# Kernel tuning notes

Hardware: AMD Instinct MI355X
Metric: run time of the kernel (lower is better)

## Reference

```python
import jax, jax.numpy as jnp
import numpy as np

B, L, D = 4, 8192, 1024

def setup_inputs() -> dict:
    key = jax.random.key(0)
    kx, kg, kc = jax.random.split(key, 3)
    scale = 1.0 / np.sqrt(D)  # ~xavier for [D,D]
    return {
        "x": jax.random.normal(kx, (B, L, D), dtype=jnp.float32),
        "Wg": jax.random.normal(kg, (D, D), dtype=jnp.float32) * scale,
        "bg": jnp.ones((D,), dtype=jnp.float32),   # gate bias init = 1.0
        "Wc": jax.random.normal(kc, (D, D), dtype=jnp.float32) * scale,
        "bc": jnp.zeros((D,), dtype=jnp.float32),  # candidate bias init = 0
    }

def _mingru_scan(gates, candidates):
    # Linear recurrence h_t = g_t * h_{t-1} + c_t, h_0 = 0, along axis=1 (L).
    # Associative combine for pairs (a, b) representing h -> a*h + b.
    def combine(e1, e2):
        a1, b1 = e1
        a2, b2 = e2
        return a2 * a1, a2 * b1 + b2
    _, h = jax.lax.associative_scan(combine, (gates, candidates), axis=1)
    return h

def reference(x, Wg, bg, Wc, bc):
    # gate_proj / candidate_proj: y = x @ W.T + b (torch Linear convention)
    gates = jax.nn.sigmoid(jnp.einsum('bld,ed->ble', x, Wg) + bg)
    candidates = jnp.tanh(jnp.einsum('bld,ed->ble', x, Wc) + bc)
    return _mingru_scan(gates, candidates)  # dropout=0 -> identity
```

## Files before the change

kernel.cpp:

```cpp
#include <hip/hip_runtime.h>
#include <math.h>

#define B_ 4
#define L_ 8192
#define D_ 1024
#define M_ (B_ * L_)
#define K_ D_

#define BM 128
#define BN 128
#define BK 32

#define NCH 64
#define CHL 128

typedef short bf16x8 __attribute__((ext_vector_type(8)));
typedef float f32x4 __attribute__((ext_vector_type(4)));

__device__ __forceinline__ unsigned short f2bf(float f) {
    unsigned u = __float_as_uint(f);
    u += 0x7fff + ((u >> 16) & 1);
    return (unsigned short)(u >> 16);
}
__device__ __forceinline__ float bf2f(unsigned short h) {
    return __uint_as_float(((unsigned)h) << 16);
}

__device__ __forceinline__ void async16(const void* g, void* l) {
    __builtin_amdgcn_global_load_lds(
        (const __attribute__((address_space(1))) unsigned int*)g,
        (__attribute__((address_space(3))) unsigned int*)l, 16, 0, 0);
}

__global__ __launch_bounds__(256) void wprep_kernel(
    const float* __restrict__ Wg, const float* __restrict__ Wc,
    unsigned short* __restrict__ Wghi, unsigned short* __restrict__ Wglo,
    unsigned short* __restrict__ Wchi, unsigned short* __restrict__ Wclo)
{
    int idx = (blockIdx.x * 256 + threadIdx.x) * 4;
    const int n = D_ * D_;
    const float* src; unsigned short *dh, *dl; int o;
    if (idx < n) { src = Wg; dh = Wghi; dl = Wglo; o = idx; }
    else         { src = Wc; dh = Wchi; dl = Wclo; o = idx - n; }
    float4 v = *(const float4*)(src + o);
    ushort4 hi, lo;
    hi.x = f2bf(v.x); lo.x = f2bf(v.x - bf2f(hi.x));
    hi.y = f2bf(v.y); lo.y = f2bf(v.y - bf2f(hi.y));
    hi.z = f2bf(v.z); lo.z = f2bf(v.z - bf2f(hi.z));
    hi.w = f2bf(v.w); lo.w = f2bf(v.w - bf2f(hi.w));
    *(ushort4*)(dh + o) = hi;
    *(ushort4*)(dl + o) = lo;
}

__global__ __launch_bounds__(256, 2) void gemm_scan_kernel(
    const float* __restrict__ X,
    const unsigned short* __restrict__ Wghi, const unsigned short* __restrict__ Wglo,
    const unsigned short* __restrict__ Wchi, const unsigned short* __restrict__ Wclo,
    const float* __restrict__ bg, const float* __restrict__ bc,
    float* __restrict__ P_ws, float* __restrict__ h_ws,
    float* __restrict__ carryA, float* __restrict__ carryB)
{
    __shared__ __align__(16) unsigned short sAhi[BM * BK];
    __shared__ __align__(16) unsigned short sAlo[BM * BK];
    __shared__ __align__(16) unsigned short sB[2][4][BN * BK];

    const int t = threadIdx.x;
    const int lane = t & 63;
    const int w = t >> 6;
    const int wrow = w >> 1;
    const int wcol = w & 1;
    const int quad = lane >> 4;
    const int l16  = lane & 15;

    const int m0 = blockIdx.x * BM;
    const int n0 = blockIdx.y * BN;

    const int rsw = (((l16 & 3) ^ ((l16 >> 2) & 3)) << 3);
    const int kq  = (quad << 3) ^ rsw;
    const int aws = ((((t >> 3) & 3) ^ ((t >> 5) & 3)) << 3);
    const int bSrcChunk = (((t & 3) ^ ((t >> 2) & 3) ^ ((t >> 4) & 3)) << 3);

    const unsigned short* const wp[4] = {Wghi, Wglo, Wchi, Wclo};

    f32x4 accg[4][4] = {};
    f32x4 accc[4][4] = {};

#pragma unroll
    for (int p = 0; p < 2; ++p) {
        const int o   = t * 16 + p * 4096;
        const int row = (t >> 2) + p * 64;
        const size_t goff = (size_t)(n0 + row) * K_ + 0 + bSrcChunk;
#pragma unroll
        for (int pl = 0; pl < 4; ++pl)
            async16(wp[pl] + goff, (char*)sB[0][pl] + o);
    }

#pragma unroll 1
    for (int s = 0; s < 32; ++s) {
        const int k0  = s * BK;
        const int cur = s & 1;

        asm volatile("" ::: "memory");
        __builtin_amdgcn_s_barrier();
        asm volatile("" ::: "memory");

        float4 xv[4];
#pragma unroll
        for (int p = 0; p < 4; ++p) {
            const int row = p * 32 + (t >> 3);
            const int k   = (t & 7) * 4;
            xv[p] = *(const float4*)(X + (size_t)(m0 + row) * K_ + k0 + k);
        }

        if (s < 31) {
#pragma unroll
            for (int p = 0; p < 2; ++p) {
                const int o   = t * 16 + p * 4096;
                const int row = (t >> 2) + p * 64;
                const size_t goff = (size_t)(n0 + row) * K_ + (k0 + BK) + bSrcChunk;
#pragma unroll
                for (int pl = 0; pl < 4; ++pl)
                    async16(wp[pl] + goff, (char*)sB[cur ^ 1][pl] + o);
            }
        }

#pragma unroll
        for (int p = 0; p < 4; ++p) {
            const int row = p * 32 + (t >> 3);
            const int kk  = ((t & 7) * 4) ^ aws;
            float4 v = xv[p];
            ushort4 hi, lo;
            hi.x = f2bf(v.x); lo.x = f2bf(v.x - bf2f(hi.x));
            hi.y = f2bf(v.y); lo.y = f2bf(v.y - bf2f(hi.y));
            hi.z = f2bf(v.z); lo.z = f2bf(v.z - bf2f(hi.z));
            hi.w = f2bf(v.w); lo.w = f2bf(v.w - bf2f(hi.w));
            *(ushort4*)(sAhi + row * BK + kk) = hi;
            *(ushort4*)(sAlo + row * BK + kk) = lo;
        }

        asm volatile("s_waitcnt lgkmcnt(0)" ::: "memory");
        asm volatile("s_waitcnt vmcnt(8)" ::: "memory");
        __builtin_amdgcn_sched_barrier(0);

        __builtin_amdgcn_s_barrier();
        asm volatile("" ::: "memory");

        const unsigned short* __restrict__ sb0 = sB[cur][0];
        const unsigned short* __restrict__ sb1 = sB[cur][1];
        const unsigned short* __restrict__ sb2 = sB[cur][2];
        const unsigned short* __restrict__ sb3 = sB[cur][3];

        bf16x8 ahi[4], alo[4];
#pragma unroll
        for (int i = 0; i < 4; ++i) {
            const int off = (wrow * 64 + i * 16 + l16) * BK + kq;
            ahi[i] = *(const bf16x8*)(sAhi + off);
            alo[i] = *(const bf16x8*)(sAlo + off);
        }
#pragma unroll
        for (int j = 0; j < 4; ++j) {
            const int off = (wcol * 64 + j * 16 + l16) * BK + kq;
            bf16x8 bgh = *(const bf16x8*)(sb0 + off);
            bf16x8 bgl = *(const bf16x8*)(sb1 + off);
            bf16x8 bch = *(const bf16x8*)(sb2 + off);
            bf16x8 bcl = *(const bf16x8*)(sb3 + off);
#pragma unroll
            for (int i = 0; i < 4; ++i) {
                accg[i][j] = __builtin_amdgcn_mfma_f32_16x16x32_bf16(ahi[i], bgh, accg[i][j], 0, 0, 0);
                accg[i][j] = __builtin_amdgcn_mfma_f32_16x16x32_bf16(ahi[i], bgl, accg[i][j], 0, 0, 0);
                accg[i][j] = __builtin_amdgcn_mfma_f32_16x16x32_bf16(alo[i], bgh, accg[i][j], 0, 0, 0);
                accc[i][j] = __builtin_amdgcn_mfma_f32_16x16x32_bf16(ahi[i], bch, accc[i][j], 0, 0, 0);
                accc[i][j] = __builtin_amdgcn_mfma_f32_16x16x32_bf16(ahi[i], bcl, accc[i][j], 0, 0, 0);
                accc[i][j] = __builtin_amdgcn_mfma_f32_16x16x32_bf16(alo[i], bch, accc[i][j], 0, 0, 0);
            }
        }
    }

    const int b   = m0 >> 13;
    const int chk = (m0 & (L_ - 1)) >> 7;

    float RunA[4], RunB[4];
#pragma unroll
    for (int j = 0; j < 4; ++j) {
        const int n = n0 + wcol * 64 + j * 16 + l16;
        const float bgv = bg[n];
        const float bcv = bc[n];
        float Ar = 1.f, Br = 0.f;
#pragma unroll
        for (int i = 0; i < 4; ++i) {
            float P[4], H[4];
            float pp = 1.f, ph = 0.f;
#pragma unroll
            for (int r = 0; r < 4; ++r) {
                float zg = accg[i][j][r] + bgv;
                float zc = accc[i][j][r] + bcv;
                float g = 1.f / (1.f + __expf(-zg));
                float c = tanhf(zc);
                float Pv = (r == 0) ? g : g * pp;
                float Hv = (r == 0) ? c : fmaf(g, ph, c);
                P[r] = Pv; H[r] = Hv; pp = Pv; ph = Hv;
            }
            float Ai = P[3], Bi = H[3];
            float A1 = __shfl(Ai, (lane - 16) & 63);
            float B1 = __shfl(Bi, (lane - 16) & 63);
            if (quad >= 1) { Bi = fmaf(Ai, B1, Bi); Ai *= A1; }
            float A2 = __shfl(Ai, (lane - 32) & 63);
            float B2 = __shfl(Bi, (lane - 32) & 63);
            if (quad >= 2) { Bi = fmaf(Ai, B2, Bi); Ai *= A2; }
            float Ae = __shfl(Ai, (lane - 16) & 63);
            float Be = __shfl(Bi, (lane - 16) & 63);
            if (quad == 0) { Ae = 1.f; Be = 0.f; }
            float Ca = Ae * Ar;
            float Cb = fmaf(Ae, Br, Be);
#pragma unroll
            for (int r = 0; r < 4; ++r) {
                float Pr = P[r];
                accg[i][j][r] = Pr * Ca;
                accc[i][j][r] = fmaf(Pr, Cb, H[r]);
            }
            float Ag  = __shfl(Ai, l16 + 48);
            float Bg2 = __shfl(Bi, l16 + 48);
            Br = fmaf(Ag, Br, Bg2);
            Ar *= Ag;
        }
        RunA[j] = Ar; RunB[j] = Br;
    }

    __syncthreads();
    float* cwf = (float*)sAhi;

    if (wrow == 0 && quad == 0) {
#pragma unroll
        for (int j = 0; j < 4; ++j) {
            cwf[(((wcol * 4 + j) * 16 + l16) << 1) + 0] = RunA[j];
            cwf[(((wcol * 4 + j) * 16 + l16) << 1) + 1] = RunB[j];
        }
    }
    __syncthreads();
    if (wrow == 1) {
#pragma unroll
        for (int j = 0; j < 4; ++j) {
            float Aw = cwf[(((wcol * 4 + j) * 16 + l16) << 1) + 0];
            float Bw = cwf[(((wcol * 4 + j) * 16 + l16) << 1) + 1];
#pragma unroll
            for (int i = 0; i < 4; ++i) {
#pragma unroll
                for (int r = 0; r < 4; ++r) {
                    float Pe = accg[i][j][r];
                    accc[i][j][r] = fmaf(Pe, Bw, accc[i][j][r]);
                    accg[i][j][r] = Pe * Aw;
                }
            }
            if (quad == 0) {
                const int n = n0 + wcol * 64 + j * 16 + l16;
                size_t co = (((size_t)b * NCH + chk) << 10) + n;
                carryA[co] = RunA[j] * Aw;
                carryB[co] = fmaf(RunA[j], Bw, RunB[j]);
            }
        }
    }

#pragma unroll
    for (int j = 0; j < 4; ++j) {
        const int n = n0 + wcol * 64 + j * 16 + l16;
#pragma unroll
        for (int i = 0; i < 4; ++i) {
#pragma unroll
            for (int r = 0; r < 4; ++r) {
                int m = m0 + wrow * 64 + i * 16 + quad * 4 + r;
                size_t o = ((size_t)m << 10) + n;
                P_ws[o] = accg[i][j][r];
                h_ws[o] = accc[i][j][r];
            }
        }
    }
}

__global__ __launch_bounds__(256) void scan_carry_kernel(
    const float* __restrict__ carryA, float* __restrict__ carryB)
{
    const int idx = blockIdx.x * 256 + threadIdx.x;
    const int b = idx >> 10;
    const int d = idx & (D_ - 1);
    float acc = 0.f;
    for (int k = 0; k < NCH; ++k) {
        const size_t o = (((size_t)b * NCH + k) << 10) + d;
        const float a  = carryA[o];
        const float bb = carryB[o];
        carryB[o] = acc;
        acc = fmaf(a, acc, bb);
    }
}

__global__ __launch_bounds__(256) void scan_apply_kernel(
    const float* __restrict__ P_ws, const float* __restrict__ h_ws,
    const float* __restrict__ carryB, float* __restrict__ out)
{
    const size_t o = ((size_t)blockIdx.x * 256 + threadIdx.x) * 4;
    const int m  = (int)(o >> 10);
    const int d  = (int)(o & (D_ - 1));
    const int b  = m >> 13;
    const int ch = (m & (L_ - 1)) >> 7;
    const float4 hin = *(const float4*)(carryB + ((((size_t)b * NCH + ch) << 10) + d));
    const float4 P = *(const float4*)(P_ws + o);
    const float4 H = *(const float4*)(h_ws + o);
    float4 r;
    r.x = fmaf(P.x, hin.x, H.x);
    r.y = fmaf(P.y, hin.y, H.y);
    r.z = fmaf(P.z, hin.z, H.z);
    r.w = fmaf(P.w, hin.w, H.w);
    *(float4*)(out + o) = r;
}

extern "C" void kernel_launch(void* const* d_in, const int* in_sizes, int n_in,
                              void* d_out, int out_size, void* d_ws, size_t ws_size,
                              hipStream_t stream)
{
    const float* x  = (const float*)d_in[0];
    const float* Wg = (const float*)d_in[1];
    const float* bg = (const float*)d_in[2];
    const float* Wc = (const float*)d_in[3];
    const float* bc = (const float*)d_in[4];
    float* out = (float*)d_out;

    float* ws = (float*)d_ws;
    float* P_ws   = ws;
    float* h_ws   = P_ws + (size_t)M_ * D_;
    float* carryA = h_ws + (size_t)M_ * D_;
    float* carryB = carryA + (size_t)B_ * NCH * D_;
    unsigned short* Wghi = (unsigned short*)(carryB + (size_t)B_ * NCH * D_);
    unsigned short* Wglo = Wghi + (size_t)D_ * D_;
    unsigned short* Wchi = Wglo + (size_t)D_ * D_;
    unsigned short* Wclo = Wchi + (size_t)D_ * D_;

    wprep_kernel<<<(2 * D_ * D_ / 4) / 256, 256, 0, stream>>>(
        Wg, Wc, Wghi, Wglo, Wchi, Wclo);

    gemm_scan_kernel<<<dim3(M_ / BM, D_ / BN), 256, 0, stream>>>(
        x, Wghi, Wglo, Wchi, Wclo, bg, bc, P_ws, h_ws, carryA, carryB);

    scan_carry_kernel<<<(B_ * D_) / 256, 256, 0, stream>>>(carryA, carryB);

    scan_apply_kernel<<<(M_ * (D_ / 4)) / 256, 256, 0, stream>>>(
        P_ws, h_ws, carryB, out);
}
```

Baseline: 696.9 us.

## Pre-split X into bf16 hi/lo planes and stream A tiles via async copies

Adds an xprep kernel that splits X into bf16 hi/lo planes once, staged in the output buffer, so the GEMM loads A tiles with async global-to-LDS copies instead of per-tile fp32 register loads plus in-loop conversion. It removes the LDS swizzles, restructures B double-buffering with pointer swaps, and raises wave priority around the MFMA block. The cost is an extra full pass over X (read 128MB, write 128MB). Dropping the swizzle may add LDS bank conflicts, and the A tile is still loaded synchronously within each iteration rather than prefetched.

```diff
diff --git a/kernel.cpp b/kernel.cpp
--- a/kernel.cpp
+++ b/kernel.cpp
@@ -52,8 +52,23 @@
     *(ushort4*)(dl + o) = lo;
 }
 
+__global__ __launch_bounds__(256) void xprep_kernel(
+    const float* __restrict__ X,
+    unsigned short* __restrict__ Xhi, unsigned short* __restrict__ Xlo)
+{
+    size_t idx = ((size_t)blockIdx.x * 256 + threadIdx.x) * 4;
+    float4 v = *(const float4*)(X + idx);
+    ushort4 hi, lo;
+    hi.x = f2bf(v.x); lo.x = f2bf(v.x - bf2f(hi.x));
+    hi.y = f2bf(v.y); lo.y = f2bf(v.y - bf2f(hi.y));
+    hi.z = f2bf(v.z); lo.z = f2bf(v.z - bf2f(hi.z));
+    hi.w = f2bf(v.w); lo.w = f2bf(v.w - bf2f(hi.w));
+    *(ushort4*)(Xhi + idx) = hi;
+    *(ushort4*)(Xlo + idx) = lo;
+}
+
 __global__ __launch_bounds__(256, 2) void gemm_scan_kernel(
-    const float* __restrict__ X,
+    const unsigned short* __restrict__ Xhi, const unsigned short* __restrict__ Xlo,
     const unsigned short* __restrict__ Wghi, const unsigned short* __restrict__ Wglo,
     const unsigned short* __restrict__ Wchi, const unsigned short* __restrict__ Wclo,
     const float* __restrict__ bg, const float* __restrict__ bc,
@@ -75,95 +90,73 @@
     const int m0 = blockIdx.x * BM;
     const int n0 = blockIdx.y * BN;
 
-    const int rsw = (((l16 & 3) ^ ((l16 >> 2) & 3)) << 3);
-    const int kq  = (quad << 3) ^ rsw;
-    const int aws = ((((t >> 3) & 3) ^ ((t >> 5) & 3)) << 3);
-    const int bSrcChunk = (((t & 3) ^ ((t >> 2) & 3) ^ ((t >> 4) & 3)) << 3);
-
-    const unsigned short* const wp[4] = {Wghi, Wglo, Wchi, Wclo};
+    const int stRow = t >> 2;
+    const int stKc  = (t & 3) << 3;
+    const int stO   = t * 16;
 
     f32x4 accg[4][4] = {};
     f32x4 accc[4][4] = {};
 
+    unsigned short* sBc = &sB[0][0][0];
+    unsigned short* sBn = &sB[1][0][0];
+
 #pragma unroll
     for (int p = 0; p < 2; ++p) {
-        const int o   = t * 16 + p * 4096;
-        const int row = (t >> 2) + p * 64;
-        const size_t goff = (size_t)(n0 + row) * K_ + 0 + bSrcChunk;
-#pragma unroll
-        for (int pl = 0; pl < 4; ++pl)
-            async16(wp[pl] + goff, (char*)sB[0][pl] + o);
+        const int o = stO + p * 4096;
+        const size_t gb = (size_t)(n0 + stRow + p * 64) * K_ + stKc;
+        async16(Wghi + gb, (char*)sBc + o);
+        async16(Wglo + gb, (char*)sBc + 8192 + o);
+        async16(Wchi + gb, (char*)sBc + 16384 + o);
+        async16(Wclo + gb, (char*)sBc + 24576 + o);
     }
 
 #pragma unroll 1
     for (int s = 0; s < 32; ++s) {
-        const int k0  = s * BK;
-        const int cur = s & 1;
-
-        asm volatile("" ::: "memory");
+        const int k0 = s * BK;
+
         __builtin_amdgcn_s_barrier();
-        asm volatile("" ::: "memory");
-
-        float4 xv[4];
-#pragma unroll
-        for (int p = 0; p < 4; ++p) {
-            const int row = p * 32 + (t >> 3);
-            const int k   = (t & 7) * 4;
-            xv[p] = *(const float4*)(X + (size_t)(m0 + row) * K_ + k0 + k);
+
+#pragma unroll
+        for (int p = 0; p < 2; ++p) {
+            const int o = stO + p * 4096;
+            const size_t ga = (size_t)(m0 + stRow + p * 64) * K_ + k0 + stKc;
+            async16(Xhi + ga, (char*)sAhi + o);
+            async16(Xlo + ga, (char*)sAlo + o);
         }
 
         if (s < 31) {
 #pragma unroll
             for (int p = 0; p < 2; ++p) {
-                const int o   = t * 16 + p * 4096;
-                const int row = (t >> 2) + p * 64;
-                const size_t goff = (size_t)(n0 + row) * K_ + (k0 + BK) + bSrcChunk;
-#pragma unroll
-                for (int pl = 0; pl < 4; ++pl)
-                    async16(wp[pl] + goff, (char*)sB[cur ^ 1][pl] + o);
-            }
-        }
-
-#pragma unroll
-        for (int p = 0; p < 4; ++p) {
-            const int row = p * 32 + (t >> 3);
-            const int kk  = ((t & 7) * 4) ^ aws;
-            float4 v = xv[p];
-            ushort4 hi, lo;
-            hi.x = f2bf(v.x); lo.x = f2bf(v.x - bf2f(hi.x));
-            hi.y = f2bf(v.y); lo.y = f2bf(v.y - bf2f(hi.y));
-            hi.z = f2bf(v.z); lo.z = f2bf(v.z - bf2f(hi.z));
-            hi.w = f2bf(v.w); lo.w = f2bf(v.w - bf2f(hi.w));
-            *(ushort4*)(sAhi + row * BK + kk) = hi;
-            *(ushort4*)(sAlo + row * BK + kk) = lo;
-        }
-
-        asm volatile("s_waitcnt lgkmcnt(0)" ::: "memory");
-        asm volatile("s_waitcnt vmcnt(8)" ::: "memory");
+                const int o = stO + p * 4096;
+                const size_t gb = (size_t)(n0 + stRow + p * 64) * K_ + (k0 + BK) + stKc;
+                async16(Wghi + gb, (char*)sBn + o);
+                async16(Wglo + gb, (char*)sBn + 8192 + o);
+                async16(Wchi + gb, (char*)sBn + 16384 + o);
+                async16(Wclo + gb, (char*)sBn + 24576 + o);
+            }
+            asm volatile("s_waitcnt vmcnt(8)" ::: "memory");
+        } else {
+            asm volatile("s_waitcnt vmcnt(0)" ::: "memory");
+        }
         __builtin_amdgcn_sched_barrier(0);
 
         __builtin_amdgcn_s_barrier();
-        asm volatile("" ::: "memory");
-
-        const unsigned short* __restrict__ sb0 = sB[cur][0];
-        const unsigned short* __restrict__ sb1 = sB[cur][1];
-        const unsigned short* __restrict__ sb2 = sB[cur][2];
-        const unsigned short* __restrict__ sb3 = sB[cur][3];
 
         bf16x8 ahi[4], alo[4];
 #pragma unroll
         for (int i = 0; i < 4; ++i) {
-            const int off = (wrow * 64 + i * 16 + l16) * BK + kq;
+            const int off = (wrow * 64 + i * 16 + l16) * BK + quad * 8;
             ahi[i] = *(const bf16x8*)(sAhi + off);
             alo[i] = *(const bf16x8*)(sAlo + off);
         }
+        __builtin_amdgcn_s_setprio(1);
 #pragma unroll
         for (int j = 0; j < 4; ++j) {
-            const int off = (wcol * 64 + j * 16 + l16) * BK + kq;
-            bf16x8 bgh = *(const bf16x8*)(sb0 + off);
-            bf16x8 bgl = *(const bf16x8*)(sb1 + off);
-            bf16x8 bch = *(const bf16x8*)(sb2 + off);
-            bf16x8 bcl = *(const bf16x8*)(sb3 + off);
+            const int off = (wcol * 64 + j * 16 + l16) * BK + quad * 8;
+            bf16x8 bgh = *(const bf16x8*)(sBc + off);
+            bf16x8 bgl = *(const bf16x8*)(sBc + 4096 + off);
+            bf16x8 bch = *(const bf16x8*)(sBc + 8192 + off);
+            bf16x8 bcl = *(const bf16x8*)(sBc + 12288 + off);
 #pragma unroll
             for (int i = 0; i < 4; ++i) {
                 accg[i][j] = __builtin_amdgcn_mfma_f32_16x16x32_bf16(ahi[i], bgh, accg[i][j], 0, 0, 0);
@@ -174,6 +167,9 @@
                 accc[i][j] = __builtin_amdgcn_mfma_f32_16x16x32_bf16(alo[i], bch, accc[i][j], 0, 0, 0);
             }
         }
+        __builtin_amdgcn_s_setprio(0);
+
+        unsigned short* tmp = sBc; sBc = sBn; sBn = tmp;
     }
 
     const int b   = m0 >> 13;
@@ -333,11 +329,16 @@
     unsigned short* Wchi = Wglo + (size_t)D_ * D_;
     unsigned short* Wclo = Wchi + (size_t)D_ * D_;
 
+    unsigned short* Xhi = (unsigned short*)out;
+    unsigned short* Xlo = Xhi + (size_t)M_ * D_;
+
     wprep_kernel<<<(2 * D_ * D_ / 4) / 256, 256, 0, stream>>>(
         Wg, Wc, Wghi, Wglo, Wchi, Wclo);
 
+    xprep_kernel<<<((size_t)M_ * D_ / 4) / 256, 256, 0, stream>>>(x, Xhi, Xlo);
+
     gemm_scan_kernel<<<dim3(M_ / BM, D_ / BN), 256, 0, stream>>>(
-        x, Wghi, Wglo, Wchi, Wclo, bg, bc, P_ws, h_ws, carryA, carryB);
+        Xhi, Xlo, Wghi, Wglo, Wchi, Wclo, bg, bc, P_ws, h_ws, carryA, carryB);
 
     scan_carry_kernel<<<(B_ * D_) / 256, 256, 0, stream>>>(carryA, carryB);
 
```

Result: slower. 727.6 us (+4.4%).
